# Optimization experiments

Measured on AMD Instinct MI355X. Metric: run time of the kernel, lower is better.

Reference implementation:

```python
import jax, jax.numpy as jnp
import numpy as np

CHUNK = 32
PRIOR = 64
POSE = 512
PRED = 128
B = 2048


def setup_inputs() -> dict:
    key = jax.random.key(0)
    k1, k2, k3, k4, k5, k6 = jax.random.split(key, 6)
    initial_feature = jax.random.normal(k1, (B, PRIOR, POSE), dtype=jnp.float32)
    pred_feature = jax.random.normal(k2, (B, PRED, POSE), dtype=jnp.float32)
    s1 = 1.0 / np.sqrt(CHUNK * POSE)
    s2 = 1.0 / np.sqrt(POSE)
    W1 = jax.random.uniform(k3, (POSE, CHUNK * POSE), minval=-s1, maxval=s1, dtype=jnp.float32)
    b1 = jax.random.uniform(k4, (POSE,), minval=-s1, maxval=s1, dtype=jnp.float32)
    W2 = jax.random.uniform(k5, (POSE, POSE), minval=-s2, maxval=s2, dtype=jnp.float32)
    b2 = jax.random.uniform(k6, (POSE,), minval=-s2, maxval=s2, dtype=jnp.float32)
    return {"initial_feature": initial_feature, "pred_feature": pred_feature,
            "W1": W1, "b1": b1, "W2": W2, "b2": b2}


def reference(initial_feature, pred_feature, W1, b1, W2, b2):
    Bn = initial_feature.shape[0]
    # last CHUNK prior frames flattened -> [B, CHUNK*POSE]
    x = initial_feature[:, PRIOR - CHUNK:, :].reshape(Bn, -1)
    # spatial_chunk_encoder (Dropout is identity in eval mode)
    mem = (x @ W1.T + b1) @ W2.T + b2          # [B, POSE]
    head = pred_feature[:, :CHUNK, :]          # [B, CHUNK, POSE]
    score = jnp.einsum('bd,bcd->bc', mem, head)  # per-token dot product
    g = jax.nn.sigmoid(score)[..., None]       # [B, CHUNK, 1]
    blended = g * head + (1.0 - g) * mem[:, None, :]
    return pred_feature.at[:, :CHUNK, :].set(blended)
```

## Files before the change

### kernel.cpp

```cpp
#include <hip/hip_runtime.h>
#include <hip/hip_bf16.h>
#include <stdint.h>

#define CHUNKC 32
#define PRIORC 64
#define POSEC 512
#define PREDC 128
#define NB 2048
#define K1 (CHUNKC*POSEC)
#define KS 8
#define KCH (K1/KS)

typedef __attribute__((ext_vector_type(8))) short bf16x8;
typedef __attribute__((ext_vector_type(8))) unsigned short u16x8;
typedef __attribute__((ext_vector_type(4))) float f32x4;
typedef __attribute__((ext_vector_type(4))) float f4v;

__device__ __forceinline__ unsigned short f2b(float f) {
    union { float f; unsigned int u; } x; x.f = f;
    unsigned int r = x.u + 0x7fffu + ((x.u >> 16) & 1u);
    return (unsigned short)(r >> 16);
}
__device__ __forceinline__ float b2f(unsigned short u) {
    union { unsigned int i; float f; } x; x.i = ((unsigned int)u) << 16; return x.f;
}
__device__ __forceinline__ unsigned short cf(float f) {
    __hip_bfloat16 h = __float2bfloat16(f);
    union { __hip_bfloat16 h; unsigned short u; } x; x.h = h; return x.u;
}

__device__ __forceinline__ void gload_lds16(const void* g, void* l) {
    __builtin_amdgcn_global_load_lds(
        (const __attribute__((address_space(1))) unsigned int*)g,
        (__attribute__((address_space(3))) unsigned int*)l, 16, 0, 0);
}

#define W1N4  2097152
#define W2N4  65536
__global__ __launch_bounds__(256) void cvt_w_kernel(const float4* __restrict__ W1,
                                                    const float4* __restrict__ W2,
                                                    ushort4* __restrict__ w1b,
                                                    ushort4* __restrict__ w2b) {
    const int64_t n = W1N4 + W2N4;
    const int64_t stride = (int64_t)gridDim.x * blockDim.x;
    for (int64_t i = (int64_t)blockIdx.x * blockDim.x + threadIdx.x; i < n; i += stride) {
        float4 v; ushort4* dst;
        if (i < W1N4) { v = W1[i]; dst = w1b + i; }
        else          { v = W2[i - W1N4]; dst = w2b + (i - W1N4); }
        *dst = make_ushort4(f2b(v.x), f2b(v.y), f2b(v.z), f2b(v.w));
    }
}

__global__ __launch_bounds__(512) void gemm1_kernel(const float* __restrict__ init,
                                                    const ushort* __restrict__ w1b,
                                                    ushort* __restrict__ part) {
    __shared__ float  As[3][128][64];
    __shared__ ushort Bs[2][256][64];
    const int t = threadIdx.x;
    const int l = t & 63, wid = t >> 6;
    const int wr = wid >> 2, wc = wid & 3;
    const int orig = (blockIdx.x & 7) * 32 + (blockIdx.x >> 3);
    const int mt = orig & 15, nt = (orig >> 4) & 1, ks = orig >> 5;
    const int NIT = KCH / 64;

    f32x4 acc[4][4] = {};

    const float*  aG = init + (int64_t)(mt * 128) * 32768 + 16384 + ks * KCH;
    const ushort* bG = w1b + (int64_t)(nt * 256) * K1 + ks * KCH;

    const int arow  = t >> 4;
    const int aslot = (t & 15) ^ ((t >> 4) & 15);
    const int brow = t >> 3;
    const int bcol = ((t & 7) ^ ((t >> 3) & 7)) * 8;

    const int fr = l & 15, fq = l >> 4;
    const int cxB = fr & 7;

    auto STAGE_A = [&](int buf, int k0) {
#pragma unroll
        for (int i = 0; i < 4; ++i)
            gload_lds16(aG + (int64_t)(i * 32 + arow) * 32768 + k0 + aslot * 4,
                        (char*)&As[buf][0][0] + i * 8192 + wid * 1024);
    };
    auto STAGE_B = [&](int buf, int k0) {
#pragma unroll
        for (int i = 0; i < 4; ++i)
            gload_lds16(bG + (int64_t)(i * 64 + brow) * K1 + k0 + bcol,
                        (char*)&Bs[buf][0][0] + i * 8192 + wid * 1024);
    };

    STAGE_A(0, 0);
    STAGE_B(0, 0);
    STAGE_A(1, 64);

    for (int it = 0; it < NIT; ++it) {
        const int ca = it % 3;
        const int cb = it & 1;
        if (it + 2 < NIT) {
            STAGE_B(cb ^ 1, (it + 1) * 64);
            STAGE_A((it + 2) % 3, (it + 2) * 64);
            asm volatile("s_waitcnt vmcnt(12)" ::: "memory");
        } else if (it + 1 < NIT) {
            STAGE_B(cb ^ 1, (it + 1) * 64);
            asm volatile("s_waitcnt vmcnt(8)" ::: "memory");
        } else {
            asm volatile("s_waitcnt vmcnt(0)" ::: "memory");
        }
        __builtin_amdgcn_s_barrier();
        asm volatile("" ::: "memory");
        __builtin_amdgcn_sched_barrier(0);
        __builtin_amdgcn_s_setprio(1);
#pragma unroll
        for (int k2 = 0; k2 < 2; ++k2) {
            bf16x8 a[4], b[4];
            const int s0 = k2 * 8 + fq * 2;
#pragma unroll
            for (int m = 0; m < 4; ++m) {
                const int r = wr * 64 + m * 16 + fr;
                f32x4 va = *(const f32x4*)&As[ca][r][((s0    ) ^ fr) * 4];
                f32x4 vb = *(const f32x4*)&As[ca][r][((s0 + 1) ^ fr) * 4];
                u16x8 w;
                w[0] = cf(va[0]); w[1] = cf(va[1]); w[2] = cf(va[2]); w[3] = cf(va[3]);
                w[4] = cf(vb[0]); w[5] = cf(vb[1]); w[6] = cf(vb[2]); w[7] = cf(vb[3]);
                union { u16x8 u; bf16x8 b; } cvtu; cvtu.u = w;
                a[m] = cvtu.b;
            }
            const int cs = ((k2 * 4 + fq) ^ cxB) * 8;
#pragma unroll
            for (int n = 0; n < 4; ++n)
                b[n] = *(const bf16x8*)&Bs[cb][wc * 64 + n * 16 + fr][cs];
#pragma unroll
            for (int m = 0; m < 4; ++m)
#pragma unroll
                for (int n = 0; n < 4; ++n)
                    acc[m][n] = __builtin_amdgcn_mfma_f32_16x16x32_bf16(a[m], b[n], acc[m][n], 0, 0, 0);
        }
        __builtin_amdgcn_s_setprio(0);
        asm volatile("" ::: "memory");
        __builtin_amdgcn_s_barrier();
    }

    ushort* P = part + (int64_t)ks * NB * POSEC;
    const int mbase = mt * 128 + wr * 64, nbase = nt * 256 + wc * 64;
#pragma unroll
    for (int m = 0; m < 4; ++m)
#pragma unroll
        for (int n = 0; n < 4; ++n) {
            int row0 = mbase + m * 16 + fq * 4;
            int col  = nbase + n * 16 + fr;
#pragma unroll
            for (int r = 0; r < 4; ++r)
                P[(int64_t)(row0 + r) * POSEC + col] = f2b(acc[m][n][r]);
        }
}

__global__ __launch_bounds__(256) void reduce_kernel(const ushort* __restrict__ part,
                                                     const float* __restrict__ b1,
                                                     u16x8* __restrict__ A2) {
    const int gid = blockIdx.x * 256 + threadIdx.x;
    const int64_t e0 = (int64_t)gid * 8;
    float s[8] = {};
#pragma unroll
    for (int k = 0; k < KS; ++k) {
        u16x8 p = *(const u16x8*)(part + (int64_t)k * (NB * POSEC) + e0);
#pragma unroll
        for (int j = 0; j < 8; ++j) s[j] += b2f(p[j]);
    }
    const int col = (int)(e0 & 511);
    f4v b0 = *(const f4v*)&b1[col];
    f4v b4 = *(const f4v*)&b1[col + 4];
    u16x8 o;
#pragma unroll
    for (int j = 0; j < 4; ++j) { o[j] = f2b(s[j] + b0[j]); o[j+4] = f2b(s[j+4] + b4[j]); }
    A2[gid] = o;
}

__global__ __launch_bounds__(256) void gemm2_kernel(const ushort* __restrict__ A2,
                                                    const ushort* __restrict__ w2b,
                                                    const float* __restrict__ b2,
                                                    float* __restrict__ mem) {
    __shared__ ushort As[64][64];
    __shared__ ushort Bs[64][64];
    const int t = threadIdx.x;
    const int l = t & 63, wid = t >> 6;
    const int wr = wid >> 1, wc = wid & 1;
    const int mt = blockIdx.x >> 3, nt = blockIdx.x & 7;

    f32x4 acc[2][2] = {};
    const ushort* aG = A2  + (int64_t)(mt * 64) * POSEC;
    const ushort* bG = w2b + (int64_t)(nt * 64) * POSEC;
    const int srow = t >> 3;
    const int scol = (((t & 7) ^ ((t >> 3) & 7))) * 8;
    const int fr = l & 15, fq = l >> 4;
    const int cx = fr & 7;

    for (int k0 = 0; k0 < POSEC; k0 += 64) {
#pragma unroll
        for (int i = 0; i < 2; ++i) {
            gload_lds16(aG + (int64_t)(i * 32 + srow) * POSEC + k0 + scol,
                        (char*)&As[0][0] + i * 4096 + wid * 1024);
            gload_lds16(bG + (int64_t)(i * 32 + srow) * POSEC + k0 + scol,
                        (char*)&Bs[0][0] + i * 4096 + wid * 1024);
        }
        __syncthreads();
#pragma unroll
        for (int k2 = 0; k2 < 2; ++k2) {
            const int cs = ((k2 * 4 + fq) ^ cx) * 8;
            bf16x8 a[2], b[2];
#pragma unroll
            for (int m = 0; m < 2; ++m)
                a[m] = *(const bf16x8*)&As[wr * 32 + m * 16 + fr][cs];
#pragma unroll
            for (int n = 0; n < 2; ++n)
                b[n] = *(const bf16x8*)&Bs[wc * 32 + n * 16 + fr][cs];
#pragma unroll
            for (int m = 0; m < 2; ++m)
#pragma unroll
                for (int n = 0; n < 2; ++n)
                    acc[m][n] = __builtin_amdgcn_mfma_f32_16x16x32_bf16(a[m], b[n], acc[m][n], 0, 0, 0);
        }
        __syncthreads();
    }

    const int mbase = mt * 64 + wr * 32, nbase = nt * 64 + wc * 32;
#pragma unroll
    for (int m = 0; m < 2; ++m)
#pragma unroll
        for (int n = 0; n < 2; ++n) {
            int row0 = mbase + m * 16 + fq * 4;
            int col  = nbase + n * 16 + fr;
            float bias = b2[col];
#pragma unroll
            for (int r = 0; r < 4; ++r)
                mem[(int64_t)(row0 + r) * POSEC + col] = acc[m][n][r] + bias;
        }
}

__global__ __launch_bounds__(256) void blend_kernel(const float* __restrict__ pred,
                                                    const float* __restrict__ mem,
                                                    float* __restrict__ out) {
    const int b = blockIdx.x;
    const int t = threadIdx.x;
    __shared__ float sm[POSEC];
    __shared__ float sg[CHUNKC];

    sm[t]       = mem[(int64_t)b * POSEC + t];
    sm[t + 256] = mem[(int64_t)b * POSEC + 256 + t];
    __syncthreads();

    const int l = t & 63, wid = t >> 6;
    const float4* sm4 = (const float4*)sm;
    const float4* p4 = (const float4*)pred + (int64_t)b * 16384;
    float4* o4 = (float4*)out + (int64_t)b * 16384;

#pragma unroll
    for (int ci = 0; ci < 8; ++ci) {
        int c = wid * 8 + ci;
        float4 h0 = p4[c * 128 + l * 2];
        float4 h1 = p4[c * 128 + l * 2 + 1];
        float4 m0 = sm4[l * 2];
        float4 m1 = sm4[l * 2 + 1];
        float s = h0.x * m0.x + h0.y * m0.y + h0.z * m0.z + h0.w * m0.w
                + h1.x * m1.x + h1.y * m1.y + h1.z * m1.z + h1.w * m1.w;
#pragma unroll
        for (int o = 32; o; o >>= 1) s += __shfl_xor(s, o);
        if (l == 0) sg[c] = 1.0f / (1.0f + expf(-s));
    }
    __syncthreads();

#pragma unroll
    for (int i = 0; i < 16; ++i) {
        int idx = i * 256 + t;
        int row = idx >> 7, c4 = idx & 127;
        float g = sg[row];
        float4 h = p4[idx];
        float4 m = sm4[c4];
        float4 r;
        r.x = g * h.x + (1.0f - g) * m.x;
        r.y = g * h.y + (1.0f - g) * m.y;
        r.z = g * h.z + (1.0f - g) * m.z;
        r.w = g * h.w + (1.0f - g) * m.w;
        o4[idx] = r;
    }
#pragma unroll
    for (int i = 0; i < 48; ++i) {
        int idx = 4096 + i * 256 + t;
        f4v h = __builtin_nontemporal_load((const f4v*)p4 + idx);
        __builtin_nontemporal_store(h, (f4v*)o4 + idx);
    }
}


extern "C" void kernel_launch(void* const* d_in, const int* in_sizes, int n_in,
                              void* d_out, int out_size, void* d_ws, size_t ws_size,
                              hipStream_t stream) {
    const float* init = (const float*)d_in[0];
    const float* pred = (const float*)d_in[1];
    const float* W1   = (const float*)d_in[2];
    const float* b1   = (const float*)d_in[3];
    const float* W2   = (const float*)d_in[4];
    const float* b2   = (const float*)d_in[5];
    float* out = (float*)d_out;

    char* ws = (char*)d_ws;
    ushort* w1b  = (ushort*)(ws);
    ushort* w2b  = (ushort*)(ws + 16777216);
    ushort* part = (ushort*)(ws + 17301504);
    ushort* A2   = (ushort*)(ws + 34078720);
    float*  mem  = (float*) (ws + 36175872);

    cvt_w_kernel<<<1024, 256, 0, stream>>>((const float4*)W1, (const float4*)W2,
                                           (ushort4*)w1b, (ushort4*)w2b);
    gemm1_kernel<<<256, 512, 0, stream>>>(init, w1b, part);
    reduce_kernel<<<512, 256, 0, stream>>>(part, b1, (u16x8*)A2);
    gemm2_kernel<<<256, 256, 0, stream>>>(A2, w2b, b2, mem);
    blend_kernel<<<NB, 256, 0, stream>>>(pred, mem, out);
}
```

Measured before the change: 289.2 us.

## Convert A tile to bf16 once via registers before LDS store in gemm1

The fp32 A tile is no longer sent directly into a triple-buffered fp32 LDS array. Each thread now loads it into registers, converts it to bf16 once, and writes a swizzled bf16 tile into a double-buffered LDS array, with two register sets alternating in a manually unrolled loop. Before, all four column-warps converted the same A fragments separately inside the MFMA phase. This removes that redundant conversion, halves A's LDS footprint and read traffic, and makes the MFMA phase pure LDS reads. The cost is extra VGPRs for the in-flight register sets and a conversion step on the critical path between the global load wait and the barrier.

```diff
diff --git a/kernel.cpp b/kernel.cpp
--- a/kernel.cpp
+++ b/kernel.cpp
@@ -10,6 +10,7 @@
 #define K1 (CHUNKC*POSEC)
 #define KS 8
 #define KCH (K1/KS)
+#define NIT (KCH/64)
 
 typedef __attribute__((ext_vector_type(8))) short bf16x8;
 typedef __attribute__((ext_vector_type(8))) unsigned short u16x8;
@@ -54,33 +55,37 @@
 __global__ __launch_bounds__(512) void gemm1_kernel(const float* __restrict__ init,
                                                     const ushort* __restrict__ w1b,
                                                     ushort* __restrict__ part) {
-    __shared__ float  As[3][128][64];
+    __shared__ ushort Ab[2][128][64];
     __shared__ ushort Bs[2][256][64];
     const int t = threadIdx.x;
     const int l = t & 63, wid = t >> 6;
     const int wr = wid >> 2, wc = wid & 3;
     const int orig = (blockIdx.x & 7) * 32 + (blockIdx.x >> 3);
     const int mt = orig & 15, nt = (orig >> 4) & 1, ks = orig >> 5;
-    const int NIT = KCH / 64;
 
     f32x4 acc[4][4] = {};
 
-    const float*  aG = init + (int64_t)(mt * 128) * 32768 + 16384 + ks * KCH;
+    const int agr = t >> 2;
+    const int agc = (t & 3) * 16;
+    const int akey = agr & 7;
+    const int as0 = (t & 3) * 2;
+    const int aw0 = (as0 ^ akey) * 8;
+    const int aw1 = ((as0 + 1) ^ akey) * 8;
+    const float* aRow = init + (int64_t)(mt * 128 + agr) * 32768 + 16384 + ks * KCH + agc;
+
     const ushort* bG = w1b + (int64_t)(nt * 256) * K1 + ks * KCH;
-
-    const int arow  = t >> 4;
-    const int aslot = (t & 15) ^ ((t >> 4) & 15);
     const int brow = t >> 3;
     const int bcol = ((t & 7) ^ ((t >> 3) & 7)) * 8;
 
     const int fr = l & 15, fq = l >> 4;
-    const int cxB = fr & 7;
-
-    auto STAGE_A = [&](int buf, int k0) {
+    const int cx = fr & 7;
+
+    f32x4 ar0[4], ar1[4];
+
+    auto AISSUE = [&](f32x4 (&set)[4], int k0) {
 #pragma unroll
         for (int i = 0; i < 4; ++i)
-            gload_lds16(aG + (int64_t)(i * 32 + arow) * 32768 + k0 + aslot * 4,
-                        (char*)&As[buf][0][0] + i * 8192 + wid * 1024);
+            set[i] = *(const f32x4*)(aRow + k0 + i * 4);
     };
     auto STAGE_B = [&](int buf, int k0) {
 #pragma unroll
@@ -88,47 +93,31 @@
             gload_lds16(bG + (int64_t)(i * 64 + brow) * K1 + k0 + bcol,
                         (char*)&Bs[buf][0][0] + i * 8192 + wid * 1024);
     };
-
-    STAGE_A(0, 0);
-    STAGE_B(0, 0);
-    STAGE_A(1, 64);
-
-    for (int it = 0; it < NIT; ++it) {
-        const int ca = it % 3;
-        const int cb = it & 1;
-        if (it + 2 < NIT) {
-            STAGE_B(cb ^ 1, (it + 1) * 64);
-            STAGE_A((it + 2) % 3, (it + 2) * 64);
-            asm volatile("s_waitcnt vmcnt(12)" ::: "memory");
-        } else if (it + 1 < NIT) {
-            STAGE_B(cb ^ 1, (it + 1) * 64);
-            asm volatile("s_waitcnt vmcnt(8)" ::: "memory");
-        } else {
-            asm volatile("s_waitcnt vmcnt(0)" ::: "memory");
-        }
+    auto CVTWRITE = [&](f32x4 (&set)[4], int buf) {
+        u16x8 w0, w1;
+#pragma unroll
+        for (int j = 0; j < 4; ++j) {
+            w0[j] = cf(set[0][j]); w0[j + 4] = cf(set[1][j]);
+            w1[j] = cf(set[2][j]); w1[j + 4] = cf(set[3][j]);
+        }
+        *(u16x8*)&Ab[buf][agr][aw0] = w0;
+        *(u16x8*)&Ab[buf][agr][aw1] = w1;
+    };
+    auto MFMA_PHASE = [&](int cur) {
         __builtin_amdgcn_s_barrier();
         asm volatile("" ::: "memory");
         __builtin_amdgcn_sched_barrier(0);
         __builtin_amdgcn_s_setprio(1);
 #pragma unroll
         for (int k2 = 0; k2 < 2; ++k2) {
+            const int cs = ((k2 * 4 + fq) ^ cx) * 8;
             bf16x8 a[4], b[4];
-            const int s0 = k2 * 8 + fq * 2;
-#pragma unroll
-            for (int m = 0; m < 4; ++m) {
-                const int r = wr * 64 + m * 16 + fr;
-                f32x4 va = *(const f32x4*)&As[ca][r][((s0    ) ^ fr) * 4];
-                f32x4 vb = *(const f32x4*)&As[ca][r][((s0 + 1) ^ fr) * 4];
-                u16x8 w;
-                w[0] = cf(va[0]); w[1] = cf(va[1]); w[2] = cf(va[2]); w[3] = cf(va[3]);
-                w[4] = cf(vb[0]); w[5] = cf(vb[1]); w[6] = cf(vb[2]); w[7] = cf(vb[3]);
-                union { u16x8 u; bf16x8 b; } cvtu; cvtu.u = w;
-                a[m] = cvtu.b;
-            }
-            const int cs = ((k2 * 4 + fq) ^ cxB) * 8;
+#pragma unroll
+            for (int m = 0; m < 4; ++m)
+                a[m] = *(const bf16x8*)&Ab[cur][wr * 64 + m * 16 + fr][cs];
 #pragma unroll
             for (int n = 0; n < 4; ++n)
-                b[n] = *(const bf16x8*)&Bs[cb][wc * 64 + n * 16 + fr][cs];
+                b[n] = *(const bf16x8*)&Bs[cur][wc * 64 + n * 16 + fr][cs];
 #pragma unroll
             for (int m = 0; m < 4; ++m)
 #pragma unroll
@@ -138,6 +127,35 @@
         __builtin_amdgcn_s_setprio(0);
         asm volatile("" ::: "memory");
         __builtin_amdgcn_s_barrier();
+    };
+    auto ITER = [&](int it, f32x4 (&cvtset)[4], f32x4 (&issueset)[4]) {
+        if (it + 2 < NIT) {
+            AISSUE(issueset, (it + 2) * 64);
+            STAGE_B((it + 1) & 1, (it + 1) * 64);
+            asm volatile("s_waitcnt vmcnt(8)" ::: "memory");
+            CVTWRITE(cvtset, (it + 1) & 1);
+            asm volatile("s_waitcnt lgkmcnt(0)" ::: "memory");
+        } else if (it + 1 < NIT) {
+            STAGE_B((it + 1) & 1, (it + 1) * 64);
+            asm volatile("s_waitcnt vmcnt(4)" ::: "memory");
+            CVTWRITE(cvtset, (it + 1) & 1);
+            asm volatile("s_waitcnt lgkmcnt(0)" ::: "memory");
+        } else {
+            asm volatile("s_waitcnt vmcnt(0)" ::: "memory");
+        }
+        MFMA_PHASE(it & 1);
+    };
+
+    AISSUE(ar0, 0);
+    AISSUE(ar1, 64);
+    STAGE_B(0, 0);
+    asm volatile("s_waitcnt vmcnt(8)" ::: "memory");
+    CVTWRITE(ar0, 0);
+
+#pragma unroll 1
+    for (int ito = 0; ito < NIT / 2; ++ito) {
+        ITER(2 * ito,     ar1, ar0);
+        ITER(2 * ito + 1, ar0, ar1);
     }
 
     ushort* P = part + (int64_t)ks * NB * POSEC;
```

Result: no change. 289.4 us (+0.1%).
